# Kernel tuning notes

Measured on AMD Instinct MI355X. Metric: run time of the kernel, lower is better.

Reference implementation:

```python
import jax, jax.numpy as jnp
import numpy as np

def setup_inputs() -> dict:
    key = jax.random.key(0)
    kq, kk, kv = jax.random.split(key, 3)
    S, D = 4096, 512
    q = jax.random.normal(kq, (S, D), dtype=jnp.float32)
    k = jax.random.normal(kk, (S, D), dtype=jnp.float32)
    v = jax.random.normal(kv, (S, D), dtype=jnp.float32)
    return {"q": q, "k": k, "v": v}

def reference(q, k, v):
    # scaled dot-product attention, unmasked (mask_future=False path)
    d = q.shape[-1]
    scores = jnp.einsum('sd,td->st', q, k) / jnp.sqrt(jnp.asarray(d, q.dtype))
    attn = jax.nn.softmax(scores, axis=-1)
    return jnp.einsum('st,td->sd', attn, v)
```

## Files before the change

### kernel.cpp

```cpp
#include <hip/hip_runtime.h>
#include <hip/hip_bf16.h>

#define SEQ 4096
#define DIM 512
#define SCALE 0.044194173824159216f

#define SPLITS 4
#define BQ 64
#define KVBLK 64
#define KEYS_PER_SPLIT (SEQ / SPLITS)
#define ITERS (KEYS_PER_SPLIT / KVBLK)
#define THR_DEFER 8.0f

typedef __attribute__((ext_vector_type(8))) short short8;
typedef __attribute__((ext_vector_type(4))) float f32x4;
typedef __attribute__((ext_vector_type(16))) float f32x16;

__device__ __forceinline__ short f2bf(float f) {
  union { float f; unsigned u; } c; c.f = f;
  unsigned u = c.u;
  return (short)((u + 0x7FFFu + ((u >> 16) & 1u)) >> 16);
}

__device__ __forceinline__ short8 pack8(float4 a, float4 b) {
  short8 r;
  r[0] = f2bf(a.x); r[1] = f2bf(a.y); r[2] = f2bf(a.z); r[3] = f2bf(a.w);
  r[4] = f2bf(b.x); r[5] = f2bf(b.y); r[6] = f2bf(b.z); r[7] = f2bf(b.w);
  return r;
}

__device__ __forceinline__ ushort4 pack4(float a, float b, float c, float d) {
  ushort4 r;
  r.x = (unsigned short)f2bf(a); r.y = (unsigned short)f2bf(b);
  r.z = (unsigned short)f2bf(c); r.w = (unsigned short)f2bf(d);
  return r;
}

__device__ __forceinline__ void gload16(const void* g, void* l) {
  __builtin_amdgcn_global_load_lds(
      (const __attribute__((address_space(1))) unsigned int*)g,
      (__attribute__((address_space(3))) unsigned int*)l, 16, 0, 0);
}

__global__ void cvt_bf16(const float* __restrict__ in, ushort* __restrict__ ob, int n8) {
  int i = blockIdx.x * blockDim.x + threadIdx.x;
  if (i >= n8) return;
  const float4* p = (const float4*)(in + (size_t)i * 8);
  short8 v = pack8(p[0], p[1]);
  *(short8*)(ob + (size_t)i * 8) = v;
}

__global__ void transpose_bf16(const float* __restrict__ v, ushort* __restrict__ vt) {
  __shared__ float t[64][65];
  const int bs = blockIdx.x % (SEQ / 64);
  const int bd = blockIdx.x / (SEQ / 64);
  const int s0 = bs * 64, d0 = bd * 64;
  const int tid = threadIdx.x;
#pragma unroll
  for (int k = 0; k < 16; ++k) {
    int idx = k * 256 + tid;
    int r = idx >> 6, c = idx & 63;
    t[r][c] = v[(size_t)(s0 + r) * DIM + d0 + c];
  }
  __syncthreads();
#pragma unroll
  for (int k = 0; k < 16; ++k) {
    int idx = k * 256 + tid;
    int dr = idx >> 6, sc = idx & 63;
    vt[(size_t)(d0 + dr) * SEQ + s0 + sc] = (ushort)f2bf(t[sc][dr]);
  }
}

__global__ __launch_bounds__(512, 2) void attn_split(
    const float* __restrict__ q, const ushort* __restrict__ kbf,
    const ushort* __restrict__ vt, float* __restrict__ opart,
    float* __restrict__ ml) {
  __shared__ __align__(16) ushort kt[KVBLK * DIM];
  __shared__ __align__(16) ushort vtt[DIM * KVBLK];
  __shared__ __align__(16) ushort p_lds[BQ * KVBLK];
  __shared__ float mx_st[2][BQ];
  __shared__ float osc_st[BQ];
  __shared__ float l_st[2][BQ];
  __shared__ int   flag_st[4];

  const int tid  = threadIdx.x;
  const int lane = tid & 63;
  const int w    = tid >> 6;
  const int lr   = lane & 15;
  const int lg   = lane >> 4;
  const int l31  = lane & 31;
  const int hi   = lane >> 5;
  const int sp   = blockIdx.x & (SPLITS - 1);
  const int qb   = blockIdx.x >> 2;
  const int rg   = w & 3;
  const int kh   = w >> 2;
  const int rg_pv = w & 1;
  const int cg    = w >> 1;
  const int qrow0 = qb * BQ;
  const int kbase = sp * KEYS_PER_SPLIT;

  short8 qf[16];
  {
    const float* qp = q + (size_t)(qrow0 + rg * 16 + lr) * DIM + lg * 8;
#pragma unroll
    for (int c = 0; c < 16; ++c)
      qf[c] = pack8(*(const float4*)(qp + c * 32), *(const float4*)(qp + c * 32 + 4));
  }
  f32x16 oacc[4] = {};
  float m_reg = -INFINITY, l_reg = 0.f;

  auto stageK = [&](int kb) {
#pragma unroll
    for (int i = 0; i < 8; ++i) {
      int r = w * 8 + i;
      const ushort* src = kbf + (size_t)(kb + r) * DIM + ((lane ^ (r & 31)) * 8);
      gload16(src, &kt[r * DIM]);
    }
  };
  auto stageV = [&](int kb) {
#pragma unroll
    for (int j = 0; j < 8; ++j) {
      int r0 = w * 64 + j * 8;
      int rr = r0 + (lane >> 3);
      const ushort* src = vt + (size_t)rr * SEQ + kb + (((lane & 7) ^ (rr & 7)) * 8);
      gload16(src, &vtt[r0 * KVBLK]);
    }
  };

  stageK(kbase);

#pragma unroll 1
  for (int it = 0; it < ITERS; ++it) {
    const int kb = kbase + it * KVBLK;

    stageV(kb);
    asm volatile("s_waitcnt vmcnt(8)" ::: "memory");
    __builtin_amdgcn_s_barrier();

    f32x4 s0 = {}, s1 = {};
    {
      const int kr0 = kh * 32 + lr;
      const int kr1 = kr0 + 16;
      const char* kb0 = (const char*)kt + kr0 * 1024;
      const char* kb1 = (const char*)kt + kr1 * 1024;
      const int sw0 = kr0 & 31, sw1 = kr1 & 31;
      __builtin_amdgcn_s_setprio(1);
#pragma unroll
      for (int c = 0; c < 16; ++c) {
        short8 k0 = *(const short8*)(kb0 + (((c * 4 + lg) ^ sw0) << 4));
        short8 k1 = *(const short8*)(kb1 + (((c * 4 + lg) ^ sw1) << 4));
        s0 = __builtin_amdgcn_mfma_f32_16x16x32_bf16(k0, qf[c], s0, 0, 0, 0);
        s1 = __builtin_amdgcn_mfma_f32_16x16x32_bf16(k1, qf[c], s1, 0, 0, 0);
      }
      __builtin_amdgcn_s_setprio(0);
    }

    float sc0[4], sc1[4];
#pragma unroll
    for (int r = 0; r < 4; ++r) { sc0[r] = s0[r] * SCALE; sc1[r] = s1[r] * SCALE; }
    float tmax = fmaxf(fmaxf(fmaxf(sc0[0], sc0[1]), fmaxf(sc0[2], sc0[3])),
                       fmaxf(fmaxf(sc1[0], sc1[1]), fmaxf(sc1[2], sc1[3])));
    tmax = fmaxf(tmax, __shfl_xor(tmax, 16));
    tmax = fmaxf(tmax, __shfl_xor(tmax, 32));
    if (lane < 16) mx_st[kh][rg * 16 + lane] = tmax;

    asm volatile("s_waitcnt lgkmcnt(0)" ::: "memory");
    __builtin_amdgcn_s_barrier();

    if (it + 1 < ITERS) stageK(kb + KVBLK);

    {
      const int row = rg * 16 + lr;
      float tmax64 = fmaxf(mx_st[0][row], mx_st[1][row]);
      bool resc = tmax64 > m_reg + THR_DEFER;
      float mnew = resc ? tmax64 : m_reg;
      float osc = __expf(m_reg - mnew);
      unsigned long long bl = __ballot(resc);
      if (kh == 0 && lane == 0) flag_st[rg] = (bl != 0ull) ? 1 : 0;
      if (kh == 0 && lane < 16) osc_st[row] = osc;
      m_reg = mnew;
      l_reg *= osc;
      float p0[4], p1[4];
#pragma unroll
      for (int r = 0; r < 4; ++r) {
        p0[r] = __expf(sc0[r] - m_reg);
        p1[r] = __expf(sc1[r] - m_reg);
      }
      float ps = ((p0[0] + p0[1]) + (p0[2] + p0[3])) +
                 ((p1[0] + p1[1]) + (p1[2] + p1[3]));
      ps += __shfl_xor(ps, 16);
      ps += __shfl_xor(ps, 32);
      l_reg += ps;
      char* pb = (char*)p_lds + row * 128;
      const int sw = (row & 7) << 4;
      const int off = kh * 64 + lg * 8;
      *(ushort4*)(pb + (off ^ sw))        = pack4(p0[0], p0[1], p0[2], p0[3]);
      *(ushort4*)(pb + ((off + 32) ^ sw)) = pack4(p1[0], p1[1], p1[2], p1[3]);
    }

    if (it + 1 < ITERS) {
      asm volatile("s_waitcnt vmcnt(8)" ::: "memory");
    } else {
      asm volatile("s_waitcnt vmcnt(0)" ::: "memory");
    }
    asm volatile("s_waitcnt lgkmcnt(0)" ::: "memory");
    __builtin_amdgcn_s_barrier();

    {
      if (flag_st[rg_pv * 2] | flag_st[rg_pv * 2 + 1]) {
        float ov[16];
#pragma unroll
        for (int r = 0; r < 16; ++r)
          ov[r] = osc_st[rg_pv * 32 + (r & 3) + 8 * (r >> 2) + 4 * hi];
#pragma unroll
        for (int t = 0; t < 4; ++t)
#pragma unroll
          for (int r = 0; r < 16; ++r) oacc[t][r] *= ov[r];
      }
      const int arow = rg_pv * 32 + l31;
      const char* prow = (const char*)p_lds + arow * 128;
      const int psw = (arow & 7) << 4;
      __builtin_amdgcn_s_setprio(1);
#pragma unroll
      for (int c = 0; c < 4; ++c) {
        short8 pa = *(const short8*)(prow + ((c * 32 + hi * 16) ^ psw));
#pragma unroll
        for (int t = 0; t < 4; ++t) {
          int vrow = cg * 128 + t * 32 + l31;
          short8 vf = *(const short8*)((const char*)vtt + vrow * 128 +
                                       ((c * 32 + hi * 16) ^ ((vrow & 7) << 4)));
          oacc[t] = __builtin_amdgcn_mfma_f32_32x32x16_bf16(pa, vf, oacc[t], 0, 0, 0);
        }
      }
      __builtin_amdgcn_s_setprio(0);
    }
    asm volatile("s_waitcnt lgkmcnt(0)" ::: "memory");
    __builtin_amdgcn_s_barrier();
  }

  if (lane < 16) {
    l_st[kh][rg * 16 + lane] = l_reg;
    if (kh == 0) mx_st[0][rg * 16 + lane] = m_reg;
  }
  __syncthreads();
  {
    float* op = opart + ((size_t)sp * SEQ + qrow0 + rg_pv * 32) * DIM + cg * 128;
#pragma unroll
    for (int t = 0; t < 4; ++t)
#pragma unroll
      for (int r = 0; r < 16; ++r) {
        int crow = (r & 3) + 8 * (r >> 2) + 4 * hi;
        op[(size_t)crow * DIM + t * 32 + l31] = oacc[t][r];
      }
  }
  if (tid < BQ) {
    size_t base = ((size_t)sp * SEQ + qrow0 + tid) * 2;
    ml[base]     = mx_st[0][tid];
    ml[base + 1] = l_st[0][tid] + l_st[1][tid];
  }
}

__global__ void combine(const float* __restrict__ opart, const float* __restrict__ ml,
                        float* __restrict__ out) {
  int gid = blockIdx.x * 256 + threadIdx.x;
  int row = gid >> 7;
  int dv  = (gid & 127) * 4;
  float m[SPLITS], l[SPLITS], wgt[SPLITS];
  float M = -INFINITY;
#pragma unroll
  for (int i = 0; i < SPLITS; ++i) {
    m[i] = ml[((size_t)i * SEQ + row) * 2];
    l[i] = ml[((size_t)i * SEQ + row) * 2 + 1];
    M = fmaxf(M, m[i]);
  }
  float L = 0.f;
#pragma unroll
  for (int i = 0; i < SPLITS; ++i) { wgt[i] = __expf(m[i] - M); L += l[i] * wgt[i]; }
  float inv = 1.f / L;
  float4 acc = {0.f, 0.f, 0.f, 0.f};
#pragma unroll
  for (int i = 0; i < SPLITS; ++i) {
    float4 o = *(const float4*)(opart + ((size_t)i * SEQ + row) * DIM + dv);
    acc.x += o.x * wgt[i]; acc.y += o.y * wgt[i];
    acc.z += o.z * wgt[i]; acc.w += o.w * wgt[i];
  }
  acc.x *= inv; acc.y *= inv; acc.z *= inv; acc.w *= inv;
  *(float4*)(out + (size_t)row * DIM + dv) = acc;
}

__global__ __launch_bounds__(512) void attn_fused_fb(
    const float* __restrict__ q, const float* __restrict__ k,
    const float* __restrict__ v, float* __restrict__ out) {
  __shared__ float s_lds[16][128];
  __shared__ __align__(16) unsigned short p_lds[16 * 128];
  __shared__ float m_st[16], l_st[16], osc_st[16];
  const int tid = threadIdx.x, lane = tid & 63, w = tid >> 6;
  const int lr = lane & 15, lg = lane >> 4, qb = blockIdx.x * 16;
  if (tid < 16) { m_st[tid] = -INFINITY; l_st[tid] = 0.f; }
  short8 qf[16];
  {
    const float* qp = q + (size_t)(qb + lr) * DIM + lg * 8;
#pragma unroll
    for (int c = 0; c < 16; ++c)
      qf[c] = pack8(*(const float4*)(qp + c * 32), *(const float4*)(qp + c * 32 + 4));
  }
  f32x4 oacc[4] = {};
  __syncthreads();
  for (int it = 0; it < SEQ / 128; ++it) {
    const int kb = it * 128;
    {
      const float* kp = k + (size_t)(kb + w * 16 + lr) * DIM + lg * 8;
      f32x4 sacc = {};
#pragma unroll
      for (int c = 0; c < 16; ++c) {
        short8 kf = pack8(*(const float4*)(kp + c * 32), *(const float4*)(kp + c * 32 + 4));
        sacc = __builtin_amdgcn_mfma_f32_16x16x32_bf16(qf[c], kf, sacc, 0, 0, 0);
      }
#pragma unroll
      for (int r = 0; r < 4; ++r) s_lds[lg * 4 + r][w * 16 + lr] = sacc[r] * SCALE;
    }
    __syncthreads();
    {
      const int srow = tid >> 5, sj = tid & 31;
      float4 sv = *(const float4*)&s_lds[srow][sj * 4];
      float tmax = fmaxf(fmaxf(sv.x, sv.y), fmaxf(sv.z, sv.w));
#pragma unroll
      for (int m = 16; m >= 1; m >>= 1) tmax = fmaxf(tmax, __shfl_xor(tmax, m));
      float mold = m_st[srow], mnew = fmaxf(mold, tmax);
      float p0 = __expf(sv.x - mnew), p1 = __expf(sv.y - mnew);
      float p2 = __expf(sv.z - mnew), p3 = __expf(sv.w - mnew);
      float psum = (p0 + p1) + (p2 + p3);
#pragma unroll
      for (int m = 16; m >= 1; m >>= 1) psum += __shfl_xor(psum, m);
      if (sj == 0) {
        float sc = __expf(mold - mnew);
        l_st[srow] = l_st[srow] * sc + psum; m_st[srow] = mnew; osc_st[srow] = sc;
      }
      ushort4 pb;
      pb.x = (unsigned short)f2bf(p0); pb.y = (unsigned short)f2bf(p1);
      pb.z = (unsigned short)f2bf(p2); pb.w = (unsigned short)f2bf(p3);
      int lin = srow * 256 + sj * 8;
      *(ushort4*)((char*)p_lds + (lin ^ ((srow & 7) << 4))) = pb;
    }
    __syncthreads();
    {
      float osc[4];
#pragma unroll
      for (int r = 0; r < 4; ++r) osc[r] = osc_st[lg * 4 + r];
#pragma unroll
      for (int ct = 0; ct < 4; ++ct)
#pragma unroll
        for (int r = 0; r < 4; ++r) oacc[ct][r] *= osc[r];
#pragma unroll
      for (int kc = 0; kc < 4; ++kc) {
        int lin = lr * 256 + (kc * 32 + 8 * lg) * 2;
        short8 pf = *(const short8*)((const char*)p_lds + (lin ^ ((lr & 7) << 4)));
        const float* vp0 = v + (size_t)(kb + kc * 32 + 8 * lg) * DIM + w * 64 + lr;
#pragma unroll
        for (int ct = 0; ct < 4; ++ct) {
          const float* vp = vp0 + ct * 16;
          short8 vf;
#pragma unroll
          for (int jj = 0; jj < 8; ++jj) vf[jj] = f2bf(vp[(size_t)jj * DIM]);
          oacc[ct] = __builtin_amdgcn_mfma_f32_16x16x32_bf16(pf, vf, oacc[ct], 0, 0, 0);
        }
      }
    }
    __syncthreads();
  }
  {
    float linv[4];
#pragma unroll
    for (int r = 0; r < 4; ++r) linv[r] = 1.f / l_st[lg * 4 + r];
#pragma unroll
    for (int ct = 0; ct < 4; ++ct)
#pragma unroll
      for (int r = 0; r < 4; ++r)
        out[(size_t)(qb + lg * 4 + r) * DIM + w * 64 + ct * 16 + lr] =
            oacc[ct][r] * linv[r];
  }
}

extern "C" void kernel_launch(void* const* d_in, const int* in_sizes, int n_in,
                              void* d_out, int out_size, void* d_ws, size_t ws_size,
                              hipStream_t stream) {
  (void)in_sizes; (void)n_in; (void)out_size;
  const float* q = (const float*)d_in[0];
  const float* k = (const float*)d_in[1];
  const float* v = (const float*)d_in[2];
  float* out = (float*)d_out;

  const size_t kbf_elems = (size_t)SEQ * DIM;
  const size_t vt_elems  = (size_t)DIM * SEQ;
  const size_t op_elems  = (size_t)SPLITS * SEQ * DIM;
  const size_t ml_elems  = (size_t)SPLITS * SEQ * 2;
  const size_t need = kbf_elems * 2 + vt_elems * 2 + op_elems * 4 + ml_elems * 4;

  if (ws_size >= need) {
    ushort* kbf  = (ushort*)d_ws;
    ushort* vtb  = kbf + kbf_elems;
    float* opart = (float*)(vtb + vt_elems);
    float* ml    = opart + op_elems;

    cvt_bf16<<<(SEQ * DIM / 8 + 255) / 256, 256, 0, stream>>>(k, kbf, SEQ * DIM / 8);
    transpose_bf16<<<(SEQ / 64) * (DIM / 64), 256, 0, stream>>>(v, vtb);
    attn_split<<<(SEQ / BQ) * SPLITS, 512, 0, stream>>>(q, kbf, vtb, opart, ml);
    combine<<<(SEQ * DIM / 4) / 256, 256, 0, stream>>>(opart, ml, out);
  } else {
    attn_fused_fb<<<SEQ / 16, 512, 0, stream>>>(q, k, v, out);
  }
}
```

Measured before the change: 86.83 us.

## Double-buffer K/V/P tiles and overlap next-block QK with current softmax and PV

Halves the KV block to 32 keys and double-buffers the K, V^T and P shared-memory tiles along with the per-block max scratch. The QK^T MFMA for block t+1 now runs in the same iteration as the softmax and PV for block t, with loads issued two blocks ahead. The swizzles change to match the narrower 32-key rows. The aim is to hide the softmax latency and global-load waits behind matrix work and to drop one barrier per iteration. The cost is twice as many iterations and barriers per key, a full vmcnt(0) wait at the top of each iteration, and more register pressure from holding the next block's scores.

```diff
diff --git a/kernel.cpp b/kernel.cpp
--- a/kernel.cpp
+++ b/kernel.cpp
@@ -7,7 +7,7 @@
 
 #define SPLITS 4
 #define BQ 64
-#define KVBLK 64
+#define KVBLK 32
 #define KEYS_PER_SPLIT (SEQ / SPLITS)
 #define ITERS (KEYS_PER_SPLIT / KVBLK)
 #define THR_DEFER 8.0f
@@ -75,10 +75,10 @@
     const float* __restrict__ q, const ushort* __restrict__ kbf,
     const ushort* __restrict__ vt, float* __restrict__ opart,
     float* __restrict__ ml) {
-  __shared__ __align__(16) ushort kt[KVBLK * DIM];
-  __shared__ __align__(16) ushort vtt[DIM * KVBLK];
-  __shared__ __align__(16) ushort p_lds[BQ * KVBLK];
-  __shared__ float mx_st[2][BQ];
+  __shared__ __align__(16) ushort kt[2][KVBLK * DIM];
+  __shared__ __align__(16) ushort vtt[2][DIM * KVBLK];
+  __shared__ __align__(16) ushort p_lds[2][BQ * KVBLK];
+  __shared__ float mx_st[2][2][BQ];
   __shared__ float osc_st[BQ];
   __shared__ float l_st[2][BQ];
   __shared__ int   flag_st[4];
@@ -109,69 +109,71 @@
   f32x16 oacc[4] = {};
   float m_reg = -INFINITY, l_reg = 0.f;
 
-  auto stageK = [&](int kb) {
-#pragma unroll
-    for (int i = 0; i < 8; ++i) {
-      int r = w * 8 + i;
+  auto stageK = [&](int kb, int buf) {
+#pragma unroll
+    for (int i = 0; i < 4; ++i) {
+      int r = w * 4 + i;
       const ushort* src = kbf + (size_t)(kb + r) * DIM + ((lane ^ (r & 31)) * 8);
-      gload16(src, &kt[r * DIM]);
+      gload16(src, &kt[buf][r * DIM]);
     }
   };
-  auto stageV = [&](int kb) {
-#pragma unroll
-    for (int j = 0; j < 8; ++j) {
-      int r0 = w * 64 + j * 8;
-      int rr = r0 + (lane >> 3);
-      const ushort* src = vt + (size_t)rr * SEQ + kb + (((lane & 7) ^ (rr & 7)) * 8);
-      gload16(src, &vtt[r0 * KVBLK]);
+  auto stageV = [&](int kb, int buf) {
+#pragma unroll
+    for (int j = 0; j < 4; ++j) {
+      int r0 = w * 64 + j * 16;
+      int rr = r0 + (lane >> 2);
+      const ushort* src = vt + (size_t)rr * SEQ + kb + (((lane & 3) ^ (rr & 3)) * 8);
+      gload16(src, &vtt[buf][r0 * KVBLK]);
     }
   };
 
-  stageK(kbase);
+  auto qk = [&](int buf) -> f32x4 {
+    const int kr = kh * 16 + lr;
+    const char* krow = (const char*)&kt[buf][kr * DIM];
+    f32x4 s = {};
+    __builtin_amdgcn_s_setprio(1);
+#pragma unroll
+    for (int c = 0; c < 16; ++c) {
+      short8 k0 = *(const short8*)(krow + (((c * 4 + lg) ^ kr) << 4));
+      s = __builtin_amdgcn_mfma_f32_16x16x32_bf16(k0, qf[c], s, 0, 0, 0);
+    }
+    __builtin_amdgcn_s_setprio(0);
+    return s;
+  };
+
+  stageK(kbase, 0);
+  stageV(kbase, 0);
+  stageK(kbase + KVBLK, 1);
+  asm volatile("s_waitcnt vmcnt(8)" ::: "memory");
+  __builtin_amdgcn_s_barrier();
+
+  float scA[4];
+  {
+    f32x4 s = qk(0);
+#pragma unroll
+    for (int r = 0; r < 4; ++r) scA[r] = s[r] * SCALE;
+    float tm = fmaxf(fmaxf(scA[0], scA[1]), fmaxf(scA[2], scA[3]));
+    tm = fmaxf(tm, __shfl_xor(tm, 16));
+    tm = fmaxf(tm, __shfl_xor(tm, 32));
+    if (lane < 16) mx_st[0][kh][rg * 16 + lane] = tm;
+  }
+  asm volatile("s_waitcnt lgkmcnt(0)" ::: "memory");
+  __builtin_amdgcn_s_barrier();
 
 #pragma unroll 1
-  for (int it = 0; it < ITERS; ++it) {
-    const int kb = kbase + it * KVBLK;
-
-    stageV(kb);
-    asm volatile("s_waitcnt vmcnt(8)" ::: "memory");
+  for (int t = 0; t < ITERS; ++t) {
+    const int cur = t & 1, nxt = cur ^ 1;
+    const bool have_next = (t + 1 < ITERS);
+
+    asm volatile("s_waitcnt vmcnt(0)" ::: "memory");
     __builtin_amdgcn_s_barrier();
 
-    f32x4 s0 = {}, s1 = {};
-    {
-      const int kr0 = kh * 32 + lr;
-      const int kr1 = kr0 + 16;
-      const char* kb0 = (const char*)kt + kr0 * 1024;
-      const char* kb1 = (const char*)kt + kr1 * 1024;
-      const int sw0 = kr0 & 31, sw1 = kr1 & 31;
-      __builtin_amdgcn_s_setprio(1);
-#pragma unroll
-      for (int c = 0; c < 16; ++c) {
-        short8 k0 = *(const short8*)(kb0 + (((c * 4 + lg) ^ sw0) << 4));
-        short8 k1 = *(const short8*)(kb1 + (((c * 4 + lg) ^ sw1) << 4));
-        s0 = __builtin_amdgcn_mfma_f32_16x16x32_bf16(k0, qf[c], s0, 0, 0, 0);
-        s1 = __builtin_amdgcn_mfma_f32_16x16x32_bf16(k1, qf[c], s1, 0, 0, 0);
-      }
-      __builtin_amdgcn_s_setprio(0);
-    }
-
-    float sc0[4], sc1[4];
-#pragma unroll
-    for (int r = 0; r < 4; ++r) { sc0[r] = s0[r] * SCALE; sc1[r] = s1[r] * SCALE; }
-    float tmax = fmaxf(fmaxf(fmaxf(sc0[0], sc0[1]), fmaxf(sc0[2], sc0[3])),
-                       fmaxf(fmaxf(sc1[0], sc1[1]), fmaxf(sc1[2], sc1[3])));
-    tmax = fmaxf(tmax, __shfl_xor(tmax, 16));
-    tmax = fmaxf(tmax, __shfl_xor(tmax, 32));
-    if (lane < 16) mx_st[kh][rg * 16 + lane] = tmax;
-
-    asm volatile("s_waitcnt lgkmcnt(0)" ::: "memory");
-    __builtin_amdgcn_s_barrier();
-
-    if (it + 1 < ITERS) stageK(kb + KVBLK);
+    f32x4 sN = {};
+    if (have_next) sN = qk(nxt);
 
     {
       const int row = rg * 16 + lr;
-      float tmax64 = fmaxf(mx_st[0][row], mx_st[1][row]);
+      float tmax64 = fmaxf(mx_st[cur][0][row], mx_st[cur][1][row]);
       bool resc = tmax64 > m_reg + THR_DEFER;
       float mnew = resc ? tmax64 : m_reg;
       float osc = __expf(m_reg - mnew);
@@ -180,29 +182,29 @@
       if (kh == 0 && lane < 16) osc_st[row] = osc;
       m_reg = mnew;
       l_reg *= osc;
-      float p0[4], p1[4];
-#pragma unroll
-      for (int r = 0; r < 4; ++r) {
-        p0[r] = __expf(sc0[r] - m_reg);
-        p1[r] = __expf(sc1[r] - m_reg);
-      }
-      float ps = ((p0[0] + p0[1]) + (p0[2] + p0[3])) +
-                 ((p1[0] + p1[1]) + (p1[2] + p1[3]));
+      float p0[4];
+#pragma unroll
+      for (int r = 0; r < 4; ++r) p0[r] = __expf(scA[r] - m_reg);
+      float ps = (p0[0] + p0[1]) + (p0[2] + p0[3]);
       ps += __shfl_xor(ps, 16);
       ps += __shfl_xor(ps, 32);
       l_reg += ps;
-      char* pb = (char*)p_lds + row * 128;
-      const int sw = (row & 7) << 4;
-      const int off = kh * 64 + lg * 8;
-      *(ushort4*)(pb + (off ^ sw))        = pack4(p0[0], p0[1], p0[2], p0[3]);
-      *(ushort4*)(pb + ((off + 32) ^ sw)) = pack4(p1[0], p1[1], p1[2], p1[3]);
-    }
-
-    if (it + 1 < ITERS) {
-      asm volatile("s_waitcnt vmcnt(8)" ::: "memory");
-    } else {
-      asm volatile("s_waitcnt vmcnt(0)" ::: "memory");
-    }
+      char* pb = (char*)&p_lds[cur][row * KVBLK];
+      *(ushort4*)(pb + ((kh * 32 + lg * 8) ^ ((row & 3) << 4))) =
+          pack4(p0[0], p0[1], p0[2], p0[3]);
+    }
+
+    if (have_next) {
+#pragma unroll
+      for (int r = 0; r < 4; ++r) scA[r] = sN[r] * SCALE;
+      float tm = fmaxf(fmaxf(scA[0], scA[1]), fmaxf(scA[2], scA[3]));
+      tm = fmaxf(tm, __shfl_xor(tm, 16));
+      tm = fmaxf(tm, __shfl_xor(tm, 32));
+      if (lane < 16) mx_st[nxt][kh][rg * 16 + lane] = tm;
+      if (t + 2 < ITERS) stageK(kbase + (t + 2) * KVBLK, cur);
+      stageV(kbase + (t + 1) * KVBLK, nxt);
+    }
+
     asm volatile("s_waitcnt lgkmcnt(0)" ::: "memory");
     __builtin_amdgcn_s_barrier();
 
@@ -213,49 +215,47 @@
         for (int r = 0; r < 16; ++r)
           ov[r] = osc_st[rg_pv * 32 + (r & 3) + 8 * (r >> 2) + 4 * hi];
 #pragma unroll
-        for (int t = 0; t < 4; ++t)
-#pragma unroll
-          for (int r = 0; r < 16; ++r) oacc[t][r] *= ov[r];
+        for (int t4 = 0; t4 < 4; ++t4)
+#pragma unroll
+          for (int r = 0; r < 16; ++r) oacc[t4][r] *= ov[r];
       }
       const int arow = rg_pv * 32 + l31;
-      const char* prow = (const char*)p_lds + arow * 128;
-      const int psw = (arow & 7) << 4;
+      const char* prow = (const char*)&p_lds[cur][arow * KVBLK];
+      const int psw = (arow & 3) << 4;
       __builtin_amdgcn_s_setprio(1);
 #pragma unroll
-      for (int c = 0; c < 4; ++c) {
+      for (int c = 0; c < 2; ++c) {
         short8 pa = *(const short8*)(prow + ((c * 32 + hi * 16) ^ psw));
 #pragma unroll
-        for (int t = 0; t < 4; ++t) {
-          int vrow = cg * 128 + t * 32 + l31;
-          short8 vf = *(const short8*)((const char*)vtt + vrow * 128 +
-                                       ((c * 32 + hi * 16) ^ ((vrow & 7) << 4)));
-          oacc[t] = __builtin_amdgcn_mfma_f32_32x32x16_bf16(pa, vf, oacc[t], 0, 0, 0);
+        for (int t4 = 0; t4 < 4; ++t4) {
+          int vrow = cg * 128 + t4 * 32 + l31;
+          short8 vf = *(const short8*)((const char*)&vtt[cur][vrow * KVBLK] +
+                                       ((c * 32 + hi * 16) ^ ((vrow & 3) << 4)));
+          oacc[t4] = __builtin_amdgcn_mfma_f32_32x32x16_bf16(pa, vf, oacc[t4], 0, 0, 0);
         }
       }
       __builtin_amdgcn_s_setprio(0);
     }
-    asm volatile("s_waitcnt lgkmcnt(0)" ::: "memory");
-    __builtin_amdgcn_s_barrier();
   }
 
   if (lane < 16) {
     l_st[kh][rg * 16 + lane] = l_reg;
-    if (kh == 0) mx_st[0][rg * 16 + lane] = m_reg;
+    if (kh == 0) mx_st[0][0][rg * 16 + lane] = m_reg;
   }
   __syncthreads();
   {
     float* op = opart + ((size_t)sp * SEQ + qrow0 + rg_pv * 32) * DIM + cg * 128;
 #pragma unroll
-    for (int t = 0; t < 4; ++t)
+    for (int t4 = 0; t4 < 4; ++t4)
 #pragma unroll
       for (int r = 0; r < 16; ++r) {
         int crow = (r & 3) + 8 * (r >> 2) + 4 * hi;
-        op[(size_t)crow * DIM + t * 32 + l31] = oacc[t][r];
+        op[(size_t)crow * DIM + t4 * 32 + l31] = oacc[t4][r];
       }
   }
   if (tid < BQ) {
     size_t base = ((size_t)sp * SEQ + qrow0 + tid) * 2;
-    ml[base]     = mx_st[0][tid];
+    ml[base]     = mx_st[0][0][tid];
     ml[base + 1] = l_st[0][tid] + l_st[1][tid];
   }
 }
```

New measurement: 97.20 us. +11.9%, slower.

## Retile PV matmul so each wave covers all rows and a 64-column slice

Applied to the files above, without the earlier changes.

Changes the PV work split across the 8 waves. Before, each wave computed 32 query rows by 128 output columns. Now each wave computes all 64 rows by 64 columns, using a 2x2 grid of 32x32 MFMA tiles. Per k-chunk this reads 2 P fragments and 2 V fragments instead of 1 P and 4 V, cutting LDS reads from 5 to 4 per 4 MFMAs. The rescale branch now checks the flags for both row groups, and the output store uses the new mapping.

```diff
diff --git a/kernel.cpp b/kernel.cpp
--- a/kernel.cpp
+++ b/kernel.cpp
@@ -94,8 +94,6 @@
   const int qb   = blockIdx.x >> 2;
   const int rg   = w & 3;
   const int kh   = w >> 2;
-  const int rg_pv = w & 1;
-  const int cg    = w >> 1;
   const int qrow0 = qb * BQ;
   const int kbase = sp * KEYS_PER_SPLIT;
 
@@ -207,31 +205,36 @@
     __builtin_amdgcn_s_barrier();
 
     {
-      if (flag_st[rg_pv * 2] | flag_st[rg_pv * 2 + 1]) {
-        float ov[16];
-#pragma unroll
-        for (int r = 0; r < 16; ++r)
-          ov[r] = osc_st[rg_pv * 32 + (r & 3) + 8 * (r >> 2) + 4 * hi];
-#pragma unroll
-        for (int t = 0; t < 4; ++t)
-#pragma unroll
-          for (int r = 0; r < 16; ++r) oacc[t][r] *= ov[r];
-      }
-      const int arow = rg_pv * 32 + l31;
-      const char* prow = (const char*)p_lds + arow * 128;
-      const int psw = (arow & 7) << 4;
+#pragma unroll
+      for (int rt = 0; rt < 2; ++rt) {
+        if (flag_st[rt * 2] | flag_st[rt * 2 + 1]) {
+          float ov[16];
+#pragma unroll
+          for (int r = 0; r < 16; ++r)
+            ov[r] = osc_st[rt * 32 + (r & 3) + 8 * (r >> 2) + 4 * hi];
+#pragma unroll
+          for (int dt = 0; dt < 2; ++dt)
+#pragma unroll
+            for (int r = 0; r < 16; ++r) oacc[rt * 2 + dt][r] *= ov[r];
+        }
+      }
       __builtin_amdgcn_s_setprio(1);
 #pragma unroll
-      for (int c = 0; c < 4; ++c) {
-        short8 pa = *(const short8*)(prow + ((c * 32 + hi * 16) ^ psw));
-#pragma unroll
-        for (int t = 0; t < 4; ++t) {
-          int vrow = cg * 128 + t * 32 + l31;
-          short8 vf = *(const short8*)((const char*)vtt + vrow * 128 +
-                                       ((c * 32 + hi * 16) ^ ((vrow & 7) << 4)));
-          oacc[t] = __builtin_amdgcn_mfma_f32_32x32x16_bf16(pa, vf, oacc[t], 0, 0, 0);
+      for (int c = 0; c < 4; ++c)
+#pragma unroll
+        for (int rt = 0; rt < 2; ++rt) {
+          const int arow = rt * 32 + l31;
+          short8 pa = *(const short8*)((const char*)p_lds + arow * 128 +
+                                       ((c * 32 + hi * 16) ^ ((arow & 7) << 4)));
+#pragma unroll
+          for (int dt = 0; dt < 2; ++dt) {
+            int vrow = w * 64 + dt * 32 + l31;
+            short8 vf = *(const short8*)((const char*)vtt + vrow * 128 +
+                                         ((c * 32 + hi * 16) ^ ((vrow & 7) << 4)));
+            oacc[rt * 2 + dt] = __builtin_amdgcn_mfma_f32_32x32x16_bf16(
+                pa, vf, oacc[rt * 2 + dt], 0, 0, 0);
+          }
         }
-      }
       __builtin_amdgcn_s_setprio(0);
     }
     asm volatile("s_waitcnt lgkmcnt(0)" ::: "memory");
@@ -244,14 +247,16 @@
   }
   __syncthreads();
   {
-    float* op = opart + ((size_t)sp * SEQ + qrow0 + rg_pv * 32) * DIM + cg * 128;
-#pragma unroll
-    for (int t = 0; t < 4; ++t)
-#pragma unroll
-      for (int r = 0; r < 16; ++r) {
-        int crow = (r & 3) + 8 * (r >> 2) + 4 * hi;
-        op[(size_t)crow * DIM + t * 32 + l31] = oacc[t][r];
-      }
+    float* op = opart + ((size_t)sp * SEQ + qrow0) * DIM + w * 64;
+#pragma unroll
+    for (int rt = 0; rt < 2; ++rt)
+#pragma unroll
+      for (int dt = 0; dt < 2; ++dt)
+#pragma unroll
+        for (int r = 0; r < 16; ++r) {
+          int crow = rt * 32 + (r & 3) + 8 * (r >> 2) + 4 * hi;
+          op[(size_t)crow * DIM + dt * 32 + l31] = oacc[rt * 2 + dt][r];
+        }
   }
   if (tid < BQ) {
     size_t base = ((size_t)sp * SEQ + qrow0 + tid) * 2;
```

Result: slower. 92.55 us (+6.6%).
